# Kernel optimization log

Measured on AMD Instinct MI355X. Metric: run time of the kernel, lower is better.

The kernel has to match this reference:

```python
import jax, jax.numpy as jnp
import numpy as np

PI = 3.141592653589793
TAU = 2.0      # tau for both rpe_lif (spikingjelly default 2.0) and act_conv (params['tau'])
V_TH = 1.0     # spikingjelly LIFNode default v_threshold
EPS = 1e-5     # LayerNorm / BatchNorm eps


@jax.custom_vjp
def atan_spike(x):
    # Heaviside forward, ATan surrogate backward (spikingjelly surrogate.ATan, alpha=2)
    return (x >= 0.0).astype(x.dtype)

def _atan_fwd(x):
    return atan_spike(x), x

def _atan_bwd(x, g):
    # (alpha/2) / (1 + ((pi/2)*alpha*x)^2) with alpha=2 -> 1/(1+(pi*x)^2)
    return (g / (1.0 + (PI * x) ** 2),)

atan_spike.defvjp(_atan_fwd, _atan_bwd)


def lif(x_seq, tau=TAU):
    """Multi-step LIF: decay_input=True, v_reset=0, hard reset, detach_reset.
    x_seq: [T, ...]; returns spikes [T, ...]."""
    def step(v, x):
        v = v + (x - v) / tau                      # neuronal charge
        s = atan_spike(v - V_TH)                   # fire
        v = v * (1.0 - jax.lax.stop_gradient(s))   # detached hard reset to 0
        return v, s
    _, spikes = jax.lax.scan(step, jnp.zeros_like(x_seq[0]), x_seq)
    return spikes


def setup_inputs() -> dict:
    key = jax.random.key(0)
    ks = jax.random.split(key, 8)
    B, L, D, T = 256, 50, 128, 4
    n_items, n_h, n_v = 100001, 8, 4
    emb = jax.random.normal(ks[0], (n_items, D), jnp.float32) * 0.5
    emb = emb.at[0].set(0.0)  # padding_idx=0
    return {
        "item_seq": jax.random.randint(ks[1], (B, L), 0, n_items, jnp.int32),
        "emb_table": emb,
        "ln_gamma": jnp.ones((D,), jnp.float32),
        "ln_beta": jnp.zeros((D,), jnp.float32),
        "conv_v_w": jax.random.normal(ks[2], (n_v, L), jnp.float32) * float(1.0 / np.sqrt(L)),
        # per-length kernels stored padded: kernel for length k=i+1 is conv_h_w[i, :, :k, :]
        "conv_h_w": jax.random.normal(ks[3], (L, n_h, L, D), jnp.float32) * 0.02,
        "bn_gamma": jnp.ones((L, n_h), jnp.float32),
        "bn_beta": jnp.zeros((L, n_h), jnp.float32),
        "fc_h_w": jax.random.normal(ks[4], (D, n_h * L), jnp.float32) * 0.05,
        "fc_h_b": jnp.zeros((D,), jnp.float32),
        "fc_v_w": jax.random.normal(ks[5], (D, n_v * D), jnp.float32) * 0.04,
        "fc_v_b": jnp.zeros((D,), jnp.float32),
        "T": 4,
    }


def reference(item_seq, emb_table, ln_gamma, ln_beta, conv_v_w, conv_h_w,
              bn_gamma, bn_beta, fc_h_w, fc_h_b, fc_v_w, fc_v_b, T):
    B, L = item_seq.shape
    D = emb_table.shape[1]
    n_h = conv_h_w.shape[1]
    n_v = conv_v_w.shape[0]

    # embedding + LayerNorm
    emb = emb_table[item_seq]                                   # [B,L,D]
    mu = emb.mean(-1, keepdims=True)
    var = emb.var(-1, keepdims=True)
    x = (emb - mu) / jnp.sqrt(var + EPS) * ln_gamma + ln_beta   # [B,L,D]

    # repeat over T and spike (rpe_lif)
    s = lif(jnp.broadcast_to(x, (T, B, L, D)))                  # binary spikes [T,B,L,D]

    # vertical conv: kernel (L,1), no bias -> collapses seq axis
    out_v = jnp.einsum('tbld,cl->tbcd', s, conv_v_w).reshape(T, B, n_v * D)

    # horizontal multi-scale convs + BN(train stats) + LIF + global max pool
    s2 = s.reshape(T * B, 1, L, D)
    pools = []
    for i in range(L):
        k = i + 1
        w = conv_h_w[i, :, :k, :][:, None]                      # [n_h,1,k,D]
        y = jax.lax.conv_general_dilated(
            s2, w, (1, 1), 'VALID',
            dimension_numbers=('NCHW', 'OIHW', 'NCHW'))[:, :, :, 0]  # [TB,n_h,L-k+1]
        m = y.mean(axis=(0, 2))                                  # BN over (T*B, spatial)
        v = y.var(axis=(0, 2))
        y = (y - m[:, None]) * (bn_gamma[i][:, None] / jnp.sqrt(v[:, None] + EPS)) + bn_beta[i][:, None]
        y = lif(y.reshape(T, B, n_h, L - k + 1))                 # [T,B,n_h,L-k+1]
        pools.append(y.max(axis=-1))                             # [T,B,n_h]
    out_h = jnp.concatenate(pools, axis=-1)                      # [T,B,n_h*L]

    out_h = (out_h @ fc_h_w.T + fc_h_b).mean(0)                  # [B,D]
    out_v = out_v.mean(0) @ fc_v_w.T + fc_v_b                    # [B,D]
    return out_h + out_v
```

## Files before the change

kernel.cpp:

```cpp
#include <hip/hip_runtime.h>

#define B_ 256
#define L_ 50
#define D_ 128
#define T_ 4
#define NH 8
#define NV 4
#define TB_ (T_*B_)
#define EPSF 1e-5f

typedef _Float16 h8 __attribute__((ext_vector_type(8)));
typedef float f4 __attribute__((ext_vector_type(4)));

typedef __attribute__((address_space(1))) const unsigned int gas_u32;
typedef __attribute__((address_space(3))) unsigned int las_u32;
#define GLOAD_LDS16(gp, lp) __builtin_amdgcn_global_load_lds((gas_u32*)(gp), (las_u32*)(lp), 16, 0, 0)

__device__ __forceinline__ float waveSum(float v) {
    #pragma unroll
    for (int o = 32; o > 0; o >>= 1) v += __shfl_down(v, o, 64);
    return v;
}

__device__ __forceinline__ size_t yoff(int i) {
    return (size_t)8192 * (size_t)(50 * i - (i * (i - 1)) / 2);
}

__global__ __launch_bounds__(256) void k0_wsplit(
        const float* __restrict__ w, _Float16* __restrict__ whl) {
    int dk = blockIdx.x, i = blockIdx.y;
    int t = threadIdx.x;
    int c = t >> 4, gd = t & 15;
    int h = c & 7;
    bool live = (i < 50) && (dk <= i);
    const float* src = w + (((size_t)i * NH + h) * L_ + dk) * D_ + gd * 8;
    h8 o;
    #pragma unroll
    for (int e = 0; e < 8; ++e) {
        float wv = live ? src[e] : 0.f;
        _Float16 hi = (_Float16)wv;
        o[e] = (c < 8) ? hi : (_Float16)((wv - (float)hi) * 1024.f);
    }
    *(h8*)(whl + (((size_t)i * 50 + dk) * 16 + c) * 128 + ((gd ^ c) & 15) * 8) = o;
}

__global__ __launch_bounds__(128) void k1_embed_ln_lif(
        const int* __restrict__ item, const float* __restrict__ tab,
        const float* __restrict__ g, const float* __restrict__ be,
        _Float16* __restrict__ s16, float* __restrict__ smean) {
    int bid = blockIdx.x;
    int b = bid / L_, l = bid % L_;
    int d = threadIdx.x;
    int wid = d >> 6, lane = d & 63;
    __shared__ float red[2];
    int it = item[b * L_ + l];
    float e = tab[(size_t)it * D_ + d];
    float sm_ = waveSum(e);
    if (lane == 0) red[wid] = sm_;
    __syncthreads();
    float mu = (red[0] + red[1]) * (1.f / 128.f);
    __syncthreads();
    float df = e - mu;
    float s2 = waveSum(df * df);
    if (lane == 0) red[wid] = s2;
    __syncthreads();
    float var = (red[0] + red[1]) * (1.f / 128.f);
    float x = df / sqrtf(var + EPSF) * g[d] + be[d];
    float v = 0.f, acc = 0.f;
    int pos = (((d >> 3) ^ l) & 15) * 8 + (d & 7);
    #pragma unroll
    for (int t = 0; t < T_; ++t) {
        v += (x - v) * 0.5f;
        float sp = (v >= 1.f) ? 1.f : 0.f;
        v *= (1.f - sp);
        s16[((size_t)(t * B_ + b) * L_ + l) * D_ + pos] = (_Float16)sp;
        acc += sp;
    }
    smean[((size_t)b * L_ + l) * D_ + d] = acc * 0.25f;
}

template<int MTG>
__global__ __launch_bounds__(512, 2) void k2u(
        const _Float16* __restrict__ s16, const _Float16* __restrict__ whl,
        float* __restrict__ y, int gbase) {
    extern __shared__ __align__(16) char lds[];
    char* Bslot = lds + 102400;
    const int NM = 2 * MTG;
    const int tbo = blockIdx.x;
    const int grp = gbase + blockIdx.y;
    const int i0 = grp * 4;
    const int kmax = i0 + 4;
    const int tid = threadIdx.x;
    const int wave = tid >> 6, lane = tid & 63;
    const int p = wave >> 1;
    const int dh = wave & 1;
    const int c_ = lane & 15, g = lane >> 4;

    {
        const float4* src = (const float4*)(s16 + (size_t)tbo * 8 * (L_ * D_));
        float4* dst = (float4*)lds;
        for (int idx = tid; idx < 6400; idx += 512) dst[idx] = src[idx];
    }
    const char* bsrc = (const char*)whl + (size_t)i0 * 50 * 4096;
    const int o0 = tid * 16, o1 = 8192 + tid * 16;
    const int sc0 = o0 >> 12, r0 = o0 & 4095;
    const int sc1 = o1 >> 12, r1 = o1 & 4095;
    const char* g0p = bsrc + (size_t)sc0 * (50 * 4096) + r0;
    const char* g1p = bsrc + (size_t)sc1 * (50 * 4096) + r1;

    float4 n0 = *(const float4*)(g0p);
    float4 n1 = *(const float4*)(g1p);
    __syncthreads();
    *(float4*)(Bslot + o0) = n0;
    *(float4*)(Bslot + o1) = n1;
    __syncthreads();

    f4 acc[4][NM];
    #pragma unroll
    for (int sc = 0; sc < 4; ++sc)
        #pragma unroll
        for (int m = 0; m < NM; ++m) { f4 z = {0.f, 0.f, 0.f, 0.f}; acc[sc][m] = z; }

    for (int dk = 0; dk < kmax; ++dk) {
        const bool more = (dk + 1 < kmax);
        float4 m0, m1;
        if (more) {
            m0 = *(const float4*)(g0p + (size_t)(dk + 1) * 4096);
            m1 = *(const float4*)(g1p + (size_t)(dk + 1) * 4096);
        }
        __builtin_amdgcn_sched_barrier(0);
        #pragma unroll
        for (int dci = 0; dci < 2; ++dci) {
            const int dc = dh * 2 + dci;
            h8 bf[4];
            #pragma unroll
            for (int sc = 0; sc < 4; ++sc)
                bf[sc] = *(const h8*)(Bslot + sc * 4096 + c_ * 256 +
                                      ((((dc << 2) + g) ^ c_) & 15) * 16);
            #pragma unroll
            for (int m = 0; m < NM; ++m) {
                const int tbL = p * 2 + (m >= MTG ? 1 : 0);
                const int jt = (m >= MTG) ? m - MTG : m;
                int l = jt * 16 + c_ + dk; if (l > 49) l = 49;
                h8 a = *(const h8*)(lds + tbL * 12800 + l * 256 +
                                    ((((dc << 2) + g) ^ l) & 15) * 16);
                #pragma unroll
                for (int sc = 0; sc < 4; ++sc)
                    acc[sc][m] = __builtin_amdgcn_mfma_f32_16x16x32_f16(a, bf[sc], acc[sc][m], 0, 0, 0);
            }
        }
        __syncthreads();
        if (more) {
            *(float4*)(Bslot + o0) = m0;
            *(float4*)(Bslot + o1) = m1;
        }
        __syncthreads();
    }

    const int STR = 2 * NM * 4 + 4;
    float* mbuf = (float*)lds;
    #pragma unroll
    for (int half = 0; half < 2; ++half) {
        __syncthreads();
        if (dh == 1) {
            float* wp = mbuf + (size_t)(p * 64 + lane) * STR;
            #pragma unroll
            for (int sc = 0; sc < 2; ++sc)
                #pragma unroll
                for (int m = 0; m < NM; ++m)
                    *(f4*)(wp + (sc * NM + m) * 4) = acc[2 * half + sc][m];
        }
        __syncthreads();
        if (dh == 0) {
            const float* rp = mbuf + (size_t)(p * 64 + lane) * STR;
            #pragma unroll
            for (int sc = 0; sc < 2; ++sc)
                #pragma unroll
                for (int m = 0; m < NM; ++m)
                    acc[2 * half + sc][m] += *(const f4*)(rp + (sc * NM + m) * 4);
        }
    }

    if (dh == 0) {
        const bool hiLane = (c_ < 8);
        const int h = c_ & 7;
        #pragma unroll
        for (int sc = 0; sc < 4; ++sc) {
            const int i = i0 + sc;
            const int J = 50 - i;
            #pragma unroll
            for (int m = 0; m < NM; ++m) {
                const int tbL = p * 2 + (m >= MTG ? 1 : 0);
                const int jt = (m >= MTG) ? m - MTG : m;
                const int tb = tbo * 8 + tbL;
                size_t yb = yoff(i) + ((size_t)tb * NH + h) * J;
                #pragma unroll
                for (int r = 0; r < 4; ++r) {
                    float lo = __shfl_xor(acc[sc][m][r], 8, 64);
                    int j = jt * 16 + g * 4 + r;
                    if (hiLane && j < J) y[yb + j] = acc[sc][m][r] + lo * (1.f / 1024.f);
                }
            }
        }
    }
}

__global__ __launch_bounds__(512, 2) void k2t(
        const _Float16* __restrict__ s16, const _Float16* __restrict__ whl,
        float* __restrict__ y) {
    extern __shared__ __align__(16) char lds[];
    char* Bslot = lds + 102400;
    const int tbo = blockIdx.x;
    const int i0 = 36 + blockIdx.y * 4;
    const int kmax = (i0 + 4 <= 50) ? (i0 + 4) : 50;
    const int tid = threadIdx.x;
    const int wave = tid >> 6, lane = tid & 63;
    const int tq = wave >> 2;
    const int dc = wave & 3;
    const int c_ = lane & 15, g = lane >> 4;

    {
        const float4* src = (const float4*)(s16 + (size_t)tbo * 8 * (L_ * D_));
        float4* dst = (float4*)lds;
        for (int idx = tid; idx < 6400; idx += 512) dst[idx] = src[idx];
    }
    const char* bsrc = (const char*)whl + (size_t)i0 * 50 * 4096;
    const int o0 = tid * 16, o1 = 8192 + tid * 16;
    const char* g0p = bsrc + (size_t)(o0 >> 12) * (50 * 4096) + (o0 & 4095);
    const char* g1p = bsrc + (size_t)(o1 >> 12) * (50 * 4096) + (o1 & 4095);
    float4 n0 = *(const float4*)(g0p);
    float4 n1 = *(const float4*)(g1p);
    __syncthreads();
    *(float4*)(Bslot + o0) = n0;
    *(float4*)(Bslot + o1) = n1;
    __syncthreads();

    f4 acc[4][4];
    #pragma unroll
    for (int sc = 0; sc < 4; ++sc)
        #pragma unroll
        for (int tt = 0; tt < 4; ++tt) { f4 z = {0.f, 0.f, 0.f, 0.f}; acc[sc][tt] = z; }

    const int boffc = c_ * 256 + ((((dc << 2) + g) ^ c_) & 15) * 16;
    for (int dk = 0; dk < kmax; ++dk) {
        const bool more = (dk + 1 < kmax);
        float4 m0, m1;
        if (more) {
            m0 = *(const float4*)(g0p + (size_t)(dk + 1) * 4096);
            m1 = *(const float4*)(g1p + (size_t)(dk + 1) * 4096);
        }
        __builtin_amdgcn_sched_barrier(0);
        h8 bf[4];
        #pragma unroll
        for (int sc = 0; sc < 4; ++sc)
            bf[sc] = *(const h8*)(Bslot + sc * 4096 + boffc);
        int l = c_ + dk; if (l > 49) l = 49;
        const int aoff = l * 256 + ((((dc << 2) + g) ^ l) & 15) * 16;
        #pragma unroll
        for (int tt = 0; tt < 4; ++tt) {
            h8 a = *(const h8*)(lds + (tq * 4 + tt) * 12800 + aoff);
            #pragma unroll
            for (int sc = 0; sc < 4; ++sc)
                acc[sc][tt] = __builtin_amdgcn_mfma_f32_16x16x32_f16(a, bf[sc], acc[sc][tt], 0, 0, 0);
        }
        __syncthreads();
        if (more) {
            *(float4*)(Bslot + o0) = m0;
            *(float4*)(Bslot + o1) = m1;
        }
        __syncthreads();
    }

    f4* mbuf = (f4*)lds;
    if (dc != 0) {
        f4* wp = mbuf + (size_t)(((dc - 1) * 2 + tq) * 16) * 64 + lane;
        #pragma unroll
        for (int sc = 0; sc < 4; ++sc)
            #pragma unroll
            for (int tt = 0; tt < 4; ++tt)
                wp[(sc * 4 + tt) * 64] = acc[sc][tt];
    }
    __syncthreads();
    if (dc == 0) {
        #pragma unroll
        for (int dd = 0; dd < 3; ++dd) {
            const f4* rp = mbuf + (size_t)((dd * 2 + tq) * 16) * 64 + lane;
            #pragma unroll
            for (int sc = 0; sc < 4; ++sc)
                #pragma unroll
                for (int tt = 0; tt < 4; ++tt)
                    acc[sc][tt] += rp[(sc * 4 + tt) * 64];
        }
        const bool hiLane = (c_ < 8);
        const int h = c_ & 7;
        #pragma unroll
        for (int sc = 0; sc < 4; ++sc) {
            const int i = i0 + sc;
            const int J = 50 - i;
            if (J <= 0) continue;
            #pragma unroll
            for (int tt = 0; tt < 4; ++tt) {
                const int tb = tbo * 8 + tq * 4 + tt;
                size_t yb = yoff(i) + ((size_t)tb * NH + h) * J;
                #pragma unroll
                for (int r = 0; r < 4; ++r) {
                    float lo = __shfl_xor(acc[sc][tt][r], 8, 64);
                    int j = g * 4 + r;
                    if (hiLane && j < J) y[yb + j] = acc[sc][tt][r] + lo * (1.f / 1024.f);
                }
            }
        }
    }
}

__global__ __launch_bounds__(256) void k3_partial(
        const float* __restrict__ y, float* __restrict__ psum) {
    int ih = blockIdx.x, ck = blockIdx.y;
    int i = ih >> 3, h = ih & 7;
    int J = 50 - i;
    size_t yb = yoff(i);
    int tid = threadIdx.x;
    int grp = tid >> 5, sub = tid & 31;
    float sm = 0.f, ss = 0.f;
    for (int tb = ck * 128 + grp; tb < (ck + 1) * 128; tb += 8) {
        const float* row = y + yb + ((size_t)tb * NH + h) * J;
        for (int j = sub; j < J; j += 32) { float v = row[j]; sm += v; ss += v * v; }
    }
    __shared__ float r1[4], r2[4];
    float a = waveSum(sm), b = waveSum(ss);
    int wid = tid >> 6, lane = tid & 63;
    if (lane == 0) { r1[wid] = a; r2[wid] = b; }
    __syncthreads();
    if (tid == 0) {
        psum[((size_t)ih * 8 + ck) * 2]     = r1[0] + r1[1] + r1[2] + r1[3];
        psum[((size_t)ih * 8 + ck) * 2 + 1] = r2[0] + r2[1] + r2[2] + r2[3];
    }
}

__global__ __launch_bounds__(256) void k3_final(
        const float* __restrict__ psum, const float* __restrict__ bng,
        float* __restrict__ statm, float* __restrict__ stats_) {
    int ih = blockIdx.x * 256 + threadIdx.x;
    if (ih >= 400) return;
    float S = 0.f, Q = 0.f;
    for (int ck = 0; ck < 8; ++ck) {
        S += psum[((size_t)ih * 8 + ck) * 2];
        Q += psum[((size_t)ih * 8 + ck) * 2 + 1];
    }
    int i = ih >> 3;
    float cnt = 1024.f * (float)(50 - i);
    float m = S / cnt;
    float var = Q / cnt - m * m; if (var < 0.f) var = 0.f;
    statm[ih] = m;
    stats_[ih] = bng[ih] / sqrtf(var + EPSF);
}

__global__ __launch_bounds__(512) void k4_bn_lif_pool(
        const float* __restrict__ y, const float* __restrict__ statm,
        const float* __restrict__ stats_, const float* __restrict__ bnb,
        float* __restrict__ ps) {
    int b = blockIdx.x, i = blockIdx.y, J = L_ - i;
    int h = threadIdx.x >> 6, lane = threadIdx.x & 63;
    int ih = i * NH + h;
    float m = statm[ih], sc = stats_[ih], bb = bnb[ih];
    size_t yb = yoff(i);
    bool valid = lane < J;
    float v = 0.f; int cnt = 0;
    #pragma unroll
    for (int t = 0; t < T_; ++t) {
        int tb = t * B_ + b;
        float yn;
        if (valid) {
            float raw = y[yb + ((size_t)tb * NH + h) * J + lane];
            yn = (raw - m) * sc + bb;
        } else yn = -1e30f;
        v += (yn - v) * 0.5f;
        bool sp = (v >= 1.f);
        if (sp) v = 0.f;
        if (__any(sp)) cnt++;
    }
    if (lane == 0) ps[(size_t)b * 400 + ih] = (float)cnt;
}

__global__ __launch_bounds__(128) void k5_final(
        const float* __restrict__ smean, const float* __restrict__ ps,
        const float* __restrict__ convv, const float* __restrict__ fchw,
        const float* __restrict__ fchb, const float* __restrict__ fcvw,
        const float* __restrict__ fcvb, float* __restrict__ out) {
    __shared__ float sm_l[L_ * D_];
    __shared__ float vm[NV * D_];
    __shared__ float ps_l[400];
    int b = blockIdx.x, tid = threadIdx.x;
    for (int idx = tid; idx < L_ * D_; idx += 128) sm_l[idx] = smean[(size_t)b * (L_ * D_) + idx];
    for (int idx = tid; idx < 400; idx += 128) ps_l[idx] = ps[(size_t)b * 400 + idx];
    __syncthreads();
    int d = tid;
    #pragma unroll
    for (int c = 0; c < NV; ++c) {
        float a = 0.f;
        for (int l = 0; l < L_; ++l) a += convv[c * L_ + l] * sm_l[l * D_ + d];
        vm[c * D_ + d] = a;
    }
    __syncthreads();
    float acc = fchb[d] + fcvb[d];
    float ah = 0.f;
    for (int ih = 0; ih < 400; ++ih) ah += ps_l[ih] * fchw[d * 400 + ih];
    acc += ah * 0.25f;
    float av = 0.f;
    for (int cd = 0; cd < NV * D_; ++cd) av += vm[cd] * fcvw[d * (NV * D_) + cd];
    acc += av;
    out[(size_t)b * D_ + d] = acc;
}

extern "C" void kernel_launch(void* const* d_in, const int* in_sizes, int n_in,
                              void* d_out, int out_size, void* d_ws, size_t ws_size,
                              hipStream_t stream) {
    const int*   item  = (const int*)d_in[0];
    const float* tab   = (const float*)d_in[1];
    const float* lng   = (const float*)d_in[2];
    const float* lnb   = (const float*)d_in[3];
    const float* convv = (const float*)d_in[4];
    const float* convh = (const float*)d_in[5];
    const float* bng   = (const float*)d_in[6];
    const float* bnb   = (const float*)d_in[7];
    const float* fchw  = (const float*)d_in[8];
    const float* fchb  = (const float*)d_in[9];
    const float* fcvw  = (const float*)d_in[10];
    const float* fcvb  = (const float*)d_in[11];
    float* out = (float*)d_out;

    char* ws = (char*)d_ws;
    _Float16* s16  = (_Float16*)(ws);
    float* smean   = (float*)(ws + 13107200LL);
    float* y       = (float*)(ws + 19660800LL);
    _Float16* whl  = (_Float16*)(ws + 61440000LL);
    float* statm   = (float*)(ws + 72089600LL);
    float* stats_  = (float*)(ws + 72091200LL);
    float* ps      = (float*)(ws + 72092800LL);
    float* psum    = (float*)(ws + 72502400LL);

    hipFuncSetAttribute(reinterpret_cast<const void*>(&k2u<4>),
        hipFuncAttributeMaxDynamicSharedMemorySize, 118784);
    hipFuncSetAttribute(reinterpret_cast<const void*>(&k2u<3>),
        hipFuncAttributeMaxDynamicSharedMemorySize, 118784);
    hipFuncSetAttribute(reinterpret_cast<const void*>(&k2u<2>),
        hipFuncAttributeMaxDynamicSharedMemorySize, 118784);
    hipFuncSetAttribute(reinterpret_cast<const void*>(&k2t),
        hipFuncAttributeMaxDynamicSharedMemorySize, 118784);

    k0_wsplit<<<dim3(50, 52), 256, 0, stream>>>(convh, whl);
    k1_embed_ln_lif<<<B_ * L_, 128, 0, stream>>>(item, tab, lng, lnb, s16, smean);
    k2u<4><<<dim3(128, 1), 512, 118784, stream>>>(s16, whl, y, 0);
    k2u<3><<<dim3(128, 4), 512, 118784, stream>>>(s16, whl, y, 1);
    k2u<2><<<dim3(128, 4), 512, 118784, stream>>>(s16, whl, y, 5);
    k2t<<<dim3(128, 4), 512, 118784, stream>>>(s16, whl, y);
    k3_partial<<<dim3(400, 8), 256, 0, stream>>>(y, psum);
    k3_final<<<dim3(2, 1), 256, 0, stream>>>(psum, bng, statm, stats_);
    k4_bn_lif_pool<<<dim3(B_, L_), 512, 0, stream>>>(y, statm, stats_, bnb, ps);
    k5_final<<<B_, 128, 0, stream>>>(smean, ps, convv, fchw, fchb, fcvw, fcvb, out);
}
```

Before: 281.7 us.

## Unify conv GEMM kernels with double-buffered weight tiles and D-split waves

```diff
diff --git a/kernel.cpp b/kernel.cpp
--- a/kernel.cpp
+++ b/kernel.cpp
@@ -11,10 +11,6 @@
 
 typedef _Float16 h8 __attribute__((ext_vector_type(8)));
 typedef float f4 __attribute__((ext_vector_type(4)));
-
-typedef __attribute__((address_space(1))) const unsigned int gas_u32;
-typedef __attribute__((address_space(3))) unsigned int las_u32;
-#define GLOAD_LDS16(gp, lp) __builtin_amdgcn_global_load_lds((gas_u32*)(gp), (las_u32*)(lp), 16, 0, 0)
 
 __device__ __forceinline__ float waveSum(float v) {
     #pragma unroll
@@ -80,138 +76,13 @@
 }
 
 template<int MTG>
-__global__ __launch_bounds__(512, 2) void k2u(
+__global__ __launch_bounds__(512, 2) void k2v(
         const _Float16* __restrict__ s16, const _Float16* __restrict__ whl,
-        float* __restrict__ y, int gbase) {
+        float* __restrict__ y, int gbase, int joff) {
     extern __shared__ __align__(16) char lds[];
-    char* Bslot = lds + 102400;
-    const int NM = 2 * MTG;
+    char* B0 = lds + 102400;
     const int tbo = blockIdx.x;
-    const int grp = gbase + blockIdx.y;
-    const int i0 = grp * 4;
-    const int kmax = i0 + 4;
-    const int tid = threadIdx.x;
-    const int wave = tid >> 6, lane = tid & 63;
-    const int p = wave >> 1;
-    const int dh = wave & 1;
-    const int c_ = lane & 15, g = lane >> 4;
-
-    {
-        const float4* src = (const float4*)(s16 + (size_t)tbo * 8 * (L_ * D_));
-        float4* dst = (float4*)lds;
-        for (int idx = tid; idx < 6400; idx += 512) dst[idx] = src[idx];
-    }
-    const char* bsrc = (const char*)whl + (size_t)i0 * 50 * 4096;
-    const int o0 = tid * 16, o1 = 8192 + tid * 16;
-    const int sc0 = o0 >> 12, r0 = o0 & 4095;
-    const int sc1 = o1 >> 12, r1 = o1 & 4095;
-    const char* g0p = bsrc + (size_t)sc0 * (50 * 4096) + r0;
-    const char* g1p = bsrc + (size_t)sc1 * (50 * 4096) + r1;
-
-    float4 n0 = *(const float4*)(g0p);
-    float4 n1 = *(const float4*)(g1p);
-    __syncthreads();
-    *(float4*)(Bslot + o0) = n0;
-    *(float4*)(Bslot + o1) = n1;
-    __syncthreads();
-
-    f4 acc[4][NM];
-    #pragma unroll
-    for (int sc = 0; sc < 4; ++sc)
-        #pragma unroll
-        for (int m = 0; m < NM; ++m) { f4 z = {0.f, 0.f, 0.f, 0.f}; acc[sc][m] = z; }
-
-    for (int dk = 0; dk < kmax; ++dk) {
-        const bool more = (dk + 1 < kmax);
-        float4 m0, m1;
-        if (more) {
-            m0 = *(const float4*)(g0p + (size_t)(dk + 1) * 4096);
-            m1 = *(const float4*)(g1p + (size_t)(dk + 1) * 4096);
-        }
-        __builtin_amdgcn_sched_barrier(0);
-        #pragma unroll
-        for (int dci = 0; dci < 2; ++dci) {
-            const int dc = dh * 2 + dci;
-            h8 bf[4];
-            #pragma unroll
-            for (int sc = 0; sc < 4; ++sc)
-                bf[sc] = *(const h8*)(Bslot + sc * 4096 + c_ * 256 +
-                                      ((((dc << 2) + g) ^ c_) & 15) * 16);
-            #pragma unroll
-            for (int m = 0; m < NM; ++m) {
-                const int tbL = p * 2 + (m >= MTG ? 1 : 0);
-                const int jt = (m >= MTG) ? m - MTG : m;
-                int l = jt * 16 + c_ + dk; if (l > 49) l = 49;
-                h8 a = *(const h8*)(lds + tbL * 12800 + l * 256 +
-                                    ((((dc << 2) + g) ^ l) & 15) * 16);
-                #pragma unroll
-                for (int sc = 0; sc < 4; ++sc)
-                    acc[sc][m] = __builtin_amdgcn_mfma_f32_16x16x32_f16(a, bf[sc], acc[sc][m], 0, 0, 0);
-            }
-        }
-        __syncthreads();
-        if (more) {
-            *(float4*)(Bslot + o0) = m0;
-            *(float4*)(Bslot + o1) = m1;
-        }
-        __syncthreads();
-    }
-
-    const int STR = 2 * NM * 4 + 4;
-    float* mbuf = (float*)lds;
-    #pragma unroll
-    for (int half = 0; half < 2; ++half) {
-        __syncthreads();
-        if (dh == 1) {
-            float* wp = mbuf + (size_t)(p * 64 + lane) * STR;
-            #pragma unroll
-            for (int sc = 0; sc < 2; ++sc)
-                #pragma unroll
-                for (int m = 0; m < NM; ++m)
-                    *(f4*)(wp + (sc * NM + m) * 4) = acc[2 * half + sc][m];
-        }
-        __syncthreads();
-        if (dh == 0) {
-            const float* rp = mbuf + (size_t)(p * 64 + lane) * STR;
-            #pragma unroll
-            for (int sc = 0; sc < 2; ++sc)
-                #pragma unroll
-                for (int m = 0; m < NM; ++m)
-                    acc[2 * half + sc][m] += *(const f4*)(rp + (sc * NM + m) * 4);
-        }
-    }
-
-    if (dh == 0) {
-        const bool hiLane = (c_ < 8);
-        const int h = c_ & 7;
-        #pragma unroll
-        for (int sc = 0; sc < 4; ++sc) {
-            const int i = i0 + sc;
-            const int J = 50 - i;
-            #pragma unroll
-            for (int m = 0; m < NM; ++m) {
-                const int tbL = p * 2 + (m >= MTG ? 1 : 0);
-                const int jt = (m >= MTG) ? m - MTG : m;
-                const int tb = tbo * 8 + tbL;
-                size_t yb = yoff(i) + ((size_t)tb * NH + h) * J;
-                #pragma unroll
-                for (int r = 0; r < 4; ++r) {
-                    float lo = __shfl_xor(acc[sc][m][r], 8, 64);
-                    int j = jt * 16 + g * 4 + r;
-                    if (hiLane && j < J) y[yb + j] = acc[sc][m][r] + lo * (1.f / 1024.f);
-                }
-            }
-        }
-    }
-}
-
-__global__ __launch_bounds__(512, 2) void k2t(
-        const _Float16* __restrict__ s16, const _Float16* __restrict__ whl,
-        float* __restrict__ y) {
-    extern __shared__ __align__(16) char lds[];
-    char* Bslot = lds + 102400;
-    const int tbo = blockIdx.x;
-    const int i0 = 36 + blockIdx.y * 4;
+    const int i0 = (gbase + blockIdx.y) * 4;
     const int kmax = (i0 + 4 <= 50) ? (i0 + 4) : 50;
     const int tid = threadIdx.x;
     const int wave = tid >> 6, lane = tid & 63;
@@ -231,15 +102,17 @@
     float4 n0 = *(const float4*)(g0p);
     float4 n1 = *(const float4*)(g1p);
     __syncthreads();
-    *(float4*)(Bslot + o0) = n0;
-    *(float4*)(Bslot + o1) = n1;
-    __syncthreads();
-
-    f4 acc[4][4];
+    *(float4*)(B0 + o0) = n0;
+    *(float4*)(B0 + o1) = n1;
+    __syncthreads();
+
+    f4 acc[4][4][MTG];
     #pragma unroll
     for (int sc = 0; sc < 4; ++sc)
         #pragma unroll
-        for (int tt = 0; tt < 4; ++tt) { f4 z = {0.f, 0.f, 0.f, 0.f}; acc[sc][tt] = z; }
+        for (int tt = 0; tt < 4; ++tt)
+            #pragma unroll
+            for (int jt = 0; jt < MTG; ++jt) { f4 z = {0.f, 0.f, 0.f, 0.f}; acc[sc][tt][jt] = z; }
 
     const int boffc = c_ * 256 + ((((dc << 2) + g) ^ c_) & 15) * 16;
     for (int dk = 0; dk < kmax; ++dk) {
@@ -250,47 +123,59 @@
             m1 = *(const float4*)(g1p + (size_t)(dk + 1) * 4096);
         }
         __builtin_amdgcn_sched_barrier(0);
+        const char* Bs = B0 + (dk & 1) * 16384;
         h8 bf[4];
         #pragma unroll
         for (int sc = 0; sc < 4; ++sc)
-            bf[sc] = *(const h8*)(Bslot + sc * 4096 + boffc);
-        int l = c_ + dk; if (l > 49) l = 49;
-        const int aoff = l * 256 + ((((dc << 2) + g) ^ l) & 15) * 16;
+            bf[sc] = *(const h8*)(Bs + sc * 4096 + boffc);
         #pragma unroll
         for (int tt = 0; tt < 4; ++tt) {
-            h8 a = *(const h8*)(lds + (tq * 4 + tt) * 12800 + aoff);
-            #pragma unroll
-            for (int sc = 0; sc < 4; ++sc)
-                acc[sc][tt] = __builtin_amdgcn_mfma_f32_16x16x32_f16(a, bf[sc], acc[sc][tt], 0, 0, 0);
+            const int tbL = tq * 4 + tt;
+            #pragma unroll
+            for (int jt = 0; jt < MTG; ++jt) {
+                int l = (joff + jt) * 16 + c_ + dk; if (l > 49) l = 49;
+                h8 a = *(const h8*)(lds + tbL * 12800 + l * 256 +
+                                    ((((dc << 2) + g) ^ l) & 15) * 16);
+                #pragma unroll
+                for (int sc = 0; sc < 4; ++sc)
+                    acc[sc][tt][jt] = __builtin_amdgcn_mfma_f32_16x16x32_f16(a, bf[sc], acc[sc][tt][jt], 0, 0, 0);
+            }
+        }
+        if (more) {
+            char* Bn = B0 + ((dk + 1) & 1) * 16384;
+            *(float4*)(Bn + o0) = m0;
+            *(float4*)(Bn + o1) = m1;
         }
         __syncthreads();
-        if (more) {
-            *(float4*)(Bslot + o0) = m0;
-            *(float4*)(Bslot + o1) = m1;
-        }
+    }
+
+    f4* mbuf = (f4*)lds;
+    #pragma unroll
+    for (int jt = 0; jt < MTG; ++jt) {
         __syncthreads();
-    }
-
-    f4* mbuf = (f4*)lds;
-    if (dc != 0) {
-        f4* wp = mbuf + (size_t)(((dc - 1) * 2 + tq) * 16) * 64 + lane;
-        #pragma unroll
-        for (int sc = 0; sc < 4; ++sc)
-            #pragma unroll
-            for (int tt = 0; tt < 4; ++tt)
-                wp[(sc * 4 + tt) * 64] = acc[sc][tt];
-    }
-    __syncthreads();
-    if (dc == 0) {
-        #pragma unroll
-        for (int dd = 0; dd < 3; ++dd) {
-            const f4* rp = mbuf + (size_t)((dd * 2 + tq) * 16) * 64 + lane;
+        if (dc != 0) {
+            f4* wp = mbuf + (size_t)(((dc - 1) * 2 + tq) * 16) * 64 + lane;
             #pragma unroll
             for (int sc = 0; sc < 4; ++sc)
                 #pragma unroll
                 for (int tt = 0; tt < 4; ++tt)
-                    acc[sc][tt] += rp[(sc * 4 + tt) * 64];
-        }
+                    wp[(sc * 4 + tt) * 64] = acc[sc][tt][jt];
+        }
+        __syncthreads();
+        if (dc == 0) {
+            #pragma unroll
+            for (int dd = 0; dd < 3; ++dd) {
+                const f4* rp = mbuf + (size_t)((dd * 2 + tq) * 16) * 64 + lane;
+                #pragma unroll
+                for (int sc = 0; sc < 4; ++sc)
+                    #pragma unroll
+                    for (int tt = 0; tt < 4; ++tt)
+                        acc[sc][tt][jt] += rp[(sc * 4 + tt) * 64];
+            }
+        }
+    }
+
+    if (dc == 0) {
         const bool hiLane = (c_ < 8);
         const int h = c_ & 7;
         #pragma unroll
@@ -303,10 +188,13 @@
                 const int tb = tbo * 8 + tq * 4 + tt;
                 size_t yb = yoff(i) + ((size_t)tb * NH + h) * J;
                 #pragma unroll
-                for (int r = 0; r < 4; ++r) {
-                    float lo = __shfl_xor(acc[sc][tt][r], 8, 64);
-                    int j = g * 4 + r;
-                    if (hiLane && j < J) y[yb + j] = acc[sc][tt][r] + lo * (1.f / 1024.f);
+                for (int jt = 0; jt < MTG; ++jt) {
+                    #pragma unroll
+                    for (int r = 0; r < 4; ++r) {
+                        float lo = __shfl_xor(acc[sc][tt][jt][r], 8, 64);
+                        int j = (joff + jt) * 16 + g * 4 + r;
+                        if (hiLane && j < J) y[yb + j] = acc[sc][tt][jt][r] + lo * (1.f / 1024.f);
+                    }
                 }
             }
         }
@@ -439,21 +327,20 @@
     float* ps      = (float*)(ws + 72092800LL);
     float* psum    = (float*)(ws + 72502400LL);
 
-    hipFuncSetAttribute(reinterpret_cast<const void*>(&k2u<4>),
-        hipFuncAttributeMaxDynamicSharedMemorySize, 118784);
-    hipFuncSetAttribute(reinterpret_cast<const void*>(&k2u<3>),
-        hipFuncAttributeMaxDynamicSharedMemorySize, 118784);
-    hipFuncSetAttribute(reinterpret_cast<const void*>(&k2u<2>),
-        hipFuncAttributeMaxDynamicSharedMemorySize, 118784);
-    hipFuncSetAttribute(reinterpret_cast<const void*>(&k2t),
-        hipFuncAttributeMaxDynamicSharedMemorySize, 118784);
+    hipFuncSetAttribute(reinterpret_cast<const void*>(&k2v<1>),
+        hipFuncAttributeMaxDynamicSharedMemorySize, 135168);
+    hipFuncSetAttribute(reinterpret_cast<const void*>(&k2v<2>),
+        hipFuncAttributeMaxDynamicSharedMemorySize, 135168);
+    hipFuncSetAttribute(reinterpret_cast<const void*>(&k2v<3>),
+        hipFuncAttributeMaxDynamicSharedMemorySize, 135168);
 
     k0_wsplit<<<dim3(50, 52), 256, 0, stream>>>(convh, whl);
     k1_embed_ln_lif<<<B_ * L_, 128, 0, stream>>>(item, tab, lng, lnb, s16, smean);
-    k2u<4><<<dim3(128, 1), 512, 118784, stream>>>(s16, whl, y, 0);
-    k2u<3><<<dim3(128, 4), 512, 118784, stream>>>(s16, whl, y, 1);
-    k2u<2><<<dim3(128, 4), 512, 118784, stream>>>(s16, whl, y, 5);
-    k2t<<<dim3(128, 4), 512, 118784, stream>>>(s16, whl, y);
+    k2v<2><<<dim3(128, 1), 512, 135168, stream>>>(s16, whl, y, 0, 0);
+    k2v<2><<<dim3(128, 1), 512, 135168, stream>>>(s16, whl, y, 0, 2);
+    k2v<3><<<dim3(128, 4), 512, 135168, stream>>>(s16, whl, y, 1, 0);
+    k2v<2><<<dim3(128, 4), 512, 135168, stream>>>(s16, whl, y, 5, 0);
+    k2v<1><<<dim3(128, 4), 512, 135168, stream>>>(s16, whl, y, 9, 0);
     k3_partial<<<dim3(400, 8), 256, 0, stream>>>(y, psum);
     k3_final<<<dim3(2, 1), 256, 0, stream>>>(psum, bng, statm, stats_);
     k4_bn_lif_pool<<<dim3(B_, L_), 512, 0, stream>>>(y, statm, stats_, bnb, ps);
```

New measurement: 320.5 us. +13.8%, slower.

## Split horizontal conv GEMM into smaller 4-tb blocks with output-tile splitting

Applied to the files above, without the earlier changes.

```diff
diff --git a/kernel.cpp b/kernel.cpp
--- a/kernel.cpp
+++ b/kernel.cpp
@@ -11,10 +11,6 @@
 
 typedef _Float16 h8 __attribute__((ext_vector_type(8)));
 typedef float f4 __attribute__((ext_vector_type(4)));
-
-typedef __attribute__((address_space(1))) const unsigned int gas_u32;
-typedef __attribute__((address_space(3))) unsigned int las_u32;
-#define GLOAD_LDS16(gp, lp) __builtin_amdgcn_global_load_lds((gas_u32*)(gp), (las_u32*)(lp), 16, 0, 0)
 
 __device__ __forceinline__ float waveSum(float v) {
     #pragma unroll
@@ -80,34 +76,34 @@
 }
 
 template<int MTG>
-__global__ __launch_bounds__(512, 2) void k2u(
+__global__ __launch_bounds__(512, 4) void k2q(
         const _Float16* __restrict__ s16, const _Float16* __restrict__ whl,
-        float* __restrict__ y, int gbase) {
+        float* __restrict__ y, int mode) {
     extern __shared__ __align__(16) char lds[];
-    char* Bslot = lds + 102400;
-    const int NM = 2 * MTG;
-    const int tbo = blockIdx.x;
-    const int grp = gbase + blockIdx.y;
+    char* Bslot = lds + 51200;
+    const int tbq = blockIdx.x;
+    int grp, joff;
+    if (mode == 0) {
+        if (blockIdx.y < 2) { grp = 0; joff = 2 * blockIdx.y; }
+        else { grp = blockIdx.y - 1; joff = 0; }
+    } else { grp = blockIdx.y + 1; joff = 2; }
     const int i0 = grp * 4;
-    const int kmax = i0 + 4;
+    const int kmax = (i0 + 4 <= 50) ? (i0 + 4) : 50;
     const int tid = threadIdx.x;
     const int wave = tid >> 6, lane = tid & 63;
-    const int p = wave >> 1;
-    const int dh = wave & 1;
+    const int tq = wave >> 2;
+    const int dc = wave & 3;
     const int c_ = lane & 15, g = lane >> 4;
 
     {
-        const float4* src = (const float4*)(s16 + (size_t)tbo * 8 * (L_ * D_));
+        const float4* src = (const float4*)(s16 + (size_t)tbq * 4 * (L_ * D_));
         float4* dst = (float4*)lds;
-        for (int idx = tid; idx < 6400; idx += 512) dst[idx] = src[idx];
-    }
-    const char* bsrc = (const char*)whl + (size_t)i0 * 50 * 4096;
+        for (int idx = tid; idx < 3200; idx += 512) dst[idx] = src[idx];
+    }
+    const char* bsrc = (const char*)whl + (size_t)i0 * 204800;
     const int o0 = tid * 16, o1 = 8192 + tid * 16;
-    const int sc0 = o0 >> 12, r0 = o0 & 4095;
-    const int sc1 = o1 >> 12, r1 = o1 & 4095;
-    const char* g0p = bsrc + (size_t)sc0 * (50 * 4096) + r0;
-    const char* g1p = bsrc + (size_t)sc1 * (50 * 4096) + r1;
-
+    const char* g0p = bsrc + (size_t)(o0 >> 12) * 204800 + (o0 & 4095);
+    const char* g1p = bsrc + (size_t)(o1 >> 12) * 204800 + (o1 & 4095);
     float4 n0 = *(const float4*)(g0p);
     float4 n1 = *(const float4*)(g1p);
     __syncthreads();
@@ -115,12 +111,15 @@
     *(float4*)(Bslot + o1) = n1;
     __syncthreads();
 
-    f4 acc[4][NM];
+    f4 acc[4][2][MTG];
     #pragma unroll
     for (int sc = 0; sc < 4; ++sc)
         #pragma unroll
-        for (int m = 0; m < NM; ++m) { f4 z = {0.f, 0.f, 0.f, 0.f}; acc[sc][m] = z; }
-
+        for (int tt = 0; tt < 2; ++tt)
+            #pragma unroll
+            for (int jt = 0; jt < MTG; ++jt) { f4 z = {0.f, 0.f, 0.f, 0.f}; acc[sc][tt][jt] = z; }
+
+    const int boffc = c_ * 256 + ((((dc << 2) + g) ^ c_) & 15) * 16;
     for (int dk = 0; dk < kmax; ++dk) {
         const bool more = (dk + 1 < kmax);
         float4 m0, m1;
@@ -129,24 +128,22 @@
             m1 = *(const float4*)(g1p + (size_t)(dk + 1) * 4096);
         }
         __builtin_amdgcn_sched_barrier(0);
-        #pragma unroll
-        for (int dci = 0; dci < 2; ++dci) {
-            const int dc = dh * 2 + dci;
-            h8 bf[4];
-            #pragma unroll
-            for (int sc = 0; sc < 4; ++sc)
-                bf[sc] = *(const h8*)(Bslot + sc * 4096 + c_ * 256 +
-                                      ((((dc << 2) + g) ^ c_) & 15) * 16);
-            #pragma unroll
-            for (int m = 0; m < NM; ++m) {
-                const int tbL = p * 2 + (m >= MTG ? 1 : 0);
-                const int jt = (m >= MTG) ? m - MTG : m;
-                int l = jt * 16 + c_ + dk; if (l > 49) l = 49;
+        h8 bf[4];
+        #pragma unroll
+        for (int sc = 0; sc < 4; ++sc)
+            bf[sc] = *(const h8*)(Bslot + sc * 4096 + boffc);
+        #pragma unroll
+        for (int tt = 0; tt < 2; ++tt) {
+            const int tbL = tq * 2 + tt;
+            #pragma unroll
+            for (int jt = 0; jt < MTG; ++jt) {
+                int l = (joff + jt) * 16 + c_ + dk; if (l > 49) l = 49;
                 h8 a = *(const h8*)(lds + tbL * 12800 + l * 256 +
                                     ((((dc << 2) + g) ^ l) & 15) * 16);
-                #pragma unroll
-                for (int sc = 0; sc < 4; ++sc)
-                    acc[sc][m] = __builtin_amdgcn_mfma_f32_16x16x32_f16(a, bf[sc], acc[sc][m], 0, 0, 0);
+                acc[0][tt][jt] = __builtin_amdgcn_mfma_f32_16x16x32_f16(a, bf[0], acc[0][tt][jt], 0, 0, 0);
+                acc[1][tt][jt] = __builtin_amdgcn_mfma_f32_16x16x32_f16(a, bf[1], acc[1][tt][jt], 0, 0, 0);
+                acc[2][tt][jt] = __builtin_amdgcn_mfma_f32_16x16x32_f16(a, bf[2], acc[2][tt][jt], 0, 0, 0);
+                acc[3][tt][jt] = __builtin_amdgcn_mfma_f32_16x16x32_f16(a, bf[3], acc[3][tt][jt], 0, 0, 0);
             }
         }
         __syncthreads();
@@ -157,48 +154,49 @@
         __syncthreads();
     }
 
-    const int STR = 2 * NM * 4 + 4;
-    float* mbuf = (float*)lds;
-    #pragma unroll
-    for (int half = 0; half < 2; ++half) {
-        __syncthreads();
-        if (dh == 1) {
-            float* wp = mbuf + (size_t)(p * 64 + lane) * STR;
-            #pragma unroll
-            for (int sc = 0; sc < 2; ++sc)
+    f4* mbuf = (f4*)Bslot;
+    #pragma unroll
+    for (int jt = 0; jt < MTG; ++jt) {
+        #pragma unroll
+        for (int sc = 0; sc < 4; ++sc) {
+            __syncthreads();
+            if (dc != 0) {
+                f4* wp = mbuf + (size_t)(((dc - 1) * 2 + tq) * 2) * 64 + lane;
+                wp[0]  = acc[sc][0][jt];
+                wp[64] = acc[sc][1][jt];
+            }
+            __syncthreads();
+            if (dc == 0) {
                 #pragma unroll
-                for (int m = 0; m < NM; ++m)
-                    *(f4*)(wp + (sc * NM + m) * 4) = acc[2 * half + sc][m];
-        }
-        __syncthreads();
-        if (dh == 0) {
-            const float* rp = mbuf + (size_t)(p * 64 + lane) * STR;
-            #pragma unroll
-            for (int sc = 0; sc < 2; ++sc)
-                #pragma unroll
-                for (int m = 0; m < NM; ++m)
-                    acc[2 * half + sc][m] += *(const f4*)(rp + (sc * NM + m) * 4);
-        }
-    }
-
-    if (dh == 0) {
+                for (int dd = 0; dd < 3; ++dd) {
+                    const f4* rp = mbuf + (size_t)((dd * 2 + tq) * 2) * 64 + lane;
+                    acc[sc][0][jt] += rp[0];
+                    acc[sc][1][jt] += rp[64];
+                }
+            }
+        }
+    }
+
+    if (dc == 0) {
         const bool hiLane = (c_ < 8);
         const int h = c_ & 7;
         #pragma unroll
         for (int sc = 0; sc < 4; ++sc) {
             const int i = i0 + sc;
             const int J = 50 - i;
-            #pragma unroll
-            for (int m = 0; m < NM; ++m) {
-                const int tbL = p * 2 + (m >= MTG ? 1 : 0);
-                const int jt = (m >= MTG) ? m - MTG : m;
-                const int tb = tbo * 8 + tbL;
+            if (J <= 0) continue;
+            #pragma unroll
+            for (int tt = 0; tt < 2; ++tt) {
+                const int tb = tbq * 4 + tq * 2 + tt;
                 size_t yb = yoff(i) + ((size_t)tb * NH + h) * J;
                 #pragma unroll
-                for (int r = 0; r < 4; ++r) {
-                    float lo = __shfl_xor(acc[sc][m][r], 8, 64);
-                    int j = jt * 16 + g * 4 + r;
-                    if (hiLane && j < J) y[yb + j] = acc[sc][m][r] + lo * (1.f / 1024.f);
+                for (int jt = 0; jt < MTG; ++jt) {
+                    #pragma unroll
+                    for (int r = 0; r < 4; ++r) {
+                        float lo = __shfl_xor(acc[sc][tt][jt][r], 8, 64);
+                        int j = (joff + jt) * 16 + g * 4 + r;
+                        if (hiLane && j < J) y[yb + j] = acc[sc][tt][jt][r] + lo * (1.f / 1024.f);
+                    }
                 }
             }
         }
@@ -224,10 +222,10 @@
         float4* dst = (float4*)lds;
         for (int idx = tid; idx < 6400; idx += 512) dst[idx] = src[idx];
     }
-    const char* bsrc = (const char*)whl + (size_t)i0 * 50 * 4096;
+    const char* bsrc = (const char*)whl + (size_t)i0 * 204800;
     const int o0 = tid * 16, o1 = 8192 + tid * 16;
-    const char* g0p = bsrc + (size_t)(o0 >> 12) * (50 * 4096) + (o0 & 4095);
-    const char* g1p = bsrc + (size_t)(o1 >> 12) * (50 * 4096) + (o1 & 4095);
+    const char* g0p = bsrc + (size_t)(o0 >> 12) * 204800 + (o0 & 4095);
+    const char* g1p = bsrc + (size_t)(o1 >> 12) * 204800 + (o1 & 4095);
     float4 n0 = *(const float4*)(g0p);
     float4 n1 = *(const float4*)(g1p);
     __syncthreads();
@@ -439,20 +437,17 @@
     float* ps      = (float*)(ws + 72092800LL);
     float* psum    = (float*)(ws + 72502400LL);
 
-    hipFuncSetAttribute(reinterpret_cast<const void*>(&k2u<4>),
-        hipFuncAttributeMaxDynamicSharedMemorySize, 118784);
-    hipFuncSetAttribute(reinterpret_cast<const void*>(&k2u<3>),
-        hipFuncAttributeMaxDynamicSharedMemorySize, 118784);
-    hipFuncSetAttribute(reinterpret_cast<const void*>(&k2u<2>),
-        hipFuncAttributeMaxDynamicSharedMemorySize, 118784);
+    hipFuncSetAttribute(reinterpret_cast<const void*>(&k2q<2>),
+        hipFuncAttributeMaxDynamicSharedMemorySize, 67584);
+    hipFuncSetAttribute(reinterpret_cast<const void*>(&k2q<1>),
+        hipFuncAttributeMaxDynamicSharedMemorySize, 67584);
     hipFuncSetAttribute(reinterpret_cast<const void*>(&k2t),
         hipFuncAttributeMaxDynamicSharedMemorySize, 118784);
 
     k0_wsplit<<<dim3(50, 52), 256, 0, stream>>>(convh, whl);
     k1_embed_ln_lif<<<B_ * L_, 128, 0, stream>>>(item, tab, lng, lnb, s16, smean);
-    k2u<4><<<dim3(128, 1), 512, 118784, stream>>>(s16, whl, y, 0);
-    k2u<3><<<dim3(128, 4), 512, 118784, stream>>>(s16, whl, y, 1);
-    k2u<2><<<dim3(128, 4), 512, 118784, stream>>>(s16, whl, y, 5);
+    k2q<2><<<dim3(256, 10), 512, 67584, stream>>>(s16, whl, y, 0);
+    k2q<1><<<dim3(256, 4), 512, 67584, stream>>>(s16, whl, y, 1);
     k2t<<<dim3(128, 4), 512, 118784, stream>>>(s16, whl, y);
     k3_partial<<<dim3(400, 8), 256, 0, stream>>>(y, psum);
     k3_final<<<dim3(2, 1), 256, 0, stream>>>(psum, bng, statm, stats_);
```

Result: slower. 289.6 us (+2.8%).
